# Kernel tuning notes

Hardware: AMD Instinct MI355X
Metric: run time of the kernel (lower is better)

Reference implementation:

```python
import jax, jax.numpy as jnp
import numpy as np

N, E, DIM_H, H = 50000, 400000, 128, 8
D = DIM_H // H  # 16


def _ln(x, g, b, eps=1e-5):
    mu = jnp.mean(x, axis=-1, keepdims=True)
    var = jnp.var(x, axis=-1, keepdims=True)
    return (x - mu) * jax.lax.rsqrt(var + eps) * g + b


def setup_inputs() -> dict:
    key = jax.random.key(0)
    ks = jax.random.split(key, 20)
    s = 1.0 / np.sqrt(DIM_H)
    lin = lambda k, i, o: jax.random.uniform(k, (i, o), jnp.float32, -s, s)
    inp = {
        "node_feature": jax.random.normal(ks[0], (N, DIM_H), jnp.float32),
        "edge_feature": jax.random.normal(ks[1], (E, DIM_H), jnp.float32),
        "Wq": lin(ks[2], DIM_H, DIM_H), "bq": jnp.zeros((DIM_H,), jnp.float32),
        "Wk": lin(ks[3], DIM_H, DIM_H), "bk": jnp.zeros((DIM_H,), jnp.float32),
        "Wv": lin(ks[4], DIM_H, DIM_H), "bv": jnp.zeros((DIM_H,), jnp.float32),
        "We": lin(ks[5], DIM_H, DIM_H), "be": jnp.zeros((DIM_H,), jnp.float32),
        "Wg": lin(ks[6], DIM_H, DIM_H), "bg": jnp.zeros((DIM_H,), jnp.float32),
        "Wo": lin(ks[7], DIM_H, DIM_H), "bo": jnp.zeros((DIM_H,), jnp.float32),
        "Woe": lin(ks[8], DIM_H, DIM_H), "boe": jnp.zeros((DIM_H,), jnp.float32),
        "ln1_g": jnp.ones((DIM_H,), jnp.float32), "ln1_b": jnp.zeros((DIM_H,), jnp.float32),
        "ln1e_g": jnp.ones((DIM_H,), jnp.float32), "ln1e_b": jnp.zeros((DIM_H,), jnp.float32),
        "ln2_g": jnp.ones((DIM_H,), jnp.float32), "ln2_b": jnp.zeros((DIM_H,), jnp.float32),
        "W1": lin(ks[9], DIM_H, 2 * DIM_H), "b1": jnp.zeros((2 * DIM_H,), jnp.float32),
        "W2": lin(ks[10], 2 * DIM_H, DIM_H) / np.sqrt(2.0), "b2": jnp.zeros((DIM_H,), jnp.float32),
        "edge_index": jax.random.randint(ks[11], (2, E), 0, N, jnp.int32),
    }
    return inp


def reference(node_feature, edge_feature, Wq, bq, Wk, bk, Wv, bv, We, be, Wg, bg,
              Wo, bo, Woe, boe, ln1_g, ln1_b, ln1e_g, ln1e_b, ln2_g, ln2_b,
              W1, b1, W2, b2, edge_index):
    x_in, e_in = node_feature, edge_feature
    src, dst = edge_index[0], edge_index[1]
    n = x_in.shape[0]

    x = _ln(x_in, ln1_g, ln1_b)
    e = _ln(e_in, ln1e_g, ln1e_b)

    # node projections -> [N, H, D]
    q = (x @ Wq + bq).reshape(n, H, D)
    k = (x @ Wk + bk).reshape(n, H, D)
    v = (x @ Wv + bv).reshape(n, H, D)
    # edge projections -> [E, H, D]
    ea = (e @ We + be).reshape(-1, H, D)
    eg = (e @ Wg + bg).reshape(-1, H, D)

    # gather along edges: [E, H, D]
    edge_q = q[dst]
    edge_k = k[src]
    edge_v = v[src] * jax.nn.sigmoid(eg)

    s_elt = edge_q * edge_k + ea                      # [E, H, D] (also edge output)
    scores = jnp.clip(jnp.sum(s_elt, axis=-1) / np.sqrt(D), -5.0, 5.0)  # [E, H]

    # scatter-softmax over destination nodes, per head
    m = jax.ops.segment_max(scores, dst, num_segments=n)      # [N, H]
    ex = jnp.exp(scores - m[dst])                             # [E, H]
    ssum = jax.ops.segment_sum(ex, dst, num_segments=n)       # [N, H]
    alpha = ex / ssum[dst]                                    # [E, H]

    # scatter-add aggregation
    out = jax.ops.segment_sum(alpha[..., None] * edge_v, dst, num_segments=n)  # [N, H, D]
    out = out.reshape(n, H * D)

    x_out = x_in + out @ Wo + bo
    e_out = e_in + s_elt.reshape(-1, H * D) @ Woe + boe

    # FFN ('Single') with pre-norm + residual
    h = _ln(x_out, ln2_g, ln2_b)
    x_out = x_out + jax.nn.relu(h @ W1 + b1) @ W2 + b2
    return x_out, e_out
```

## Files before the change

kernel.cpp:

```cpp
#include <hip/hip_runtime.h>

#define NN 50000
#define NE 400000
#define CAP 64
#define PACKN (7*16384 + 32768 + 32768)
#define PACKN2 (PACKN + 32768)
#define PACKB ((PACKN2 + 255)/256)

typedef unsigned int u32;
typedef unsigned short u16;
typedef __attribute__((ext_vector_type(8))) short short8;
typedef __attribute__((ext_vector_type(4))) float f32x4;
typedef __attribute__((ext_vector_type(4))) unsigned int u32x4;

union FragU { uint4 u; short8 s; };
union Chunk { uint4 v[4]; u32 d[16]; };

__device__ __forceinline__ float bflo(u32 w){ union{u32 i; float f;} v; v.i = w<<16; return v.f; }
__device__ __forceinline__ float bfhi(u32 w){ union{u32 i; float f;} v; v.i = w & 0xffff0000u; return v.f; }
__device__ __forceinline__ u32 packbf(float a, float b){
  union{float f;u32 i;} x, y; x.f=a; y.f=b;
  u32 xi = x.i + (((x.i>>16)&1u) + 0x7fffu);
  u32 yi = y.i + (((y.i>>16)&1u) + 0x7fffu);
  return (xi>>16) | (yi & 0xffff0000u);
}

#define BAR() do { \
  asm volatile("s_waitcnt lgkmcnt(0)" ::: "memory"); \
  __builtin_amdgcn_s_barrier(); \
  asm volatile("" ::: "memory"); \
} while(0)

__device__ __forceinline__ int swz64(int row, int cp){ return row*64 + (cp ^ ((row&7)<<2)); }

__device__ __forceinline__ void stage_ln(const float* __restrict__ src, long base, long nrows,
                                         const float* __restrict__ gam, const float* __restrict__ bet,
                                         u32* __restrict__ tile, int t)
{
  int row = t>>2, sub = t&3;
  bool valid = (base + row) < nrows;
  const float* p = src + (base+row)*128 + sub*32;
  float4 x[8];
  float s=0.f, s2=0.f;
  #pragma unroll
  for(int q=0;q<8;++q){
    x[q] = valid ? *(const float4*)(p + 4*q) : make_float4(0.f,0.f,0.f,0.f);
    s  += x[q].x + x[q].y + x[q].z + x[q].w;
    s2 += x[q].x*x[q].x + x[q].y*x[q].y + x[q].z*x[q].z + x[q].w*x[q].w;
  }
  s  += __shfl_xor(s,1);  s  += __shfl_xor(s,2);
  s2 += __shfl_xor(s2,1); s2 += __shfl_xor(s2,2);
  float mu  = s*(1.f/128.f);
  float var = fmaxf(s2*(1.f/128.f) - mu*mu, 0.f);
  float rs  = rsqrtf(var + 1e-5f);
  const float* gp = gam + sub*32; const float* bp = bet + sub*32;
  #pragma unroll
  for(int m4=0;m4<4;++m4){
    float4 g0 = *(const float4*)(gp + 8*m4);
    float4 g1 = *(const float4*)(gp + 8*m4 + 4);
    float4 b0 = *(const float4*)(bp + 8*m4);
    float4 b1 = *(const float4*)(bp + 8*m4 + 4);
    float4 xa = x[2*m4], xb = x[2*m4+1];
    uint4 wv;
    wv.x = packbf((xa.x-mu)*rs*g0.x+b0.x, (xa.y-mu)*rs*g0.y+b0.y);
    wv.y = packbf((xa.z-mu)*rs*g0.z+b0.z, (xa.w-mu)*rs*g0.w+b0.w);
    wv.z = packbf((xb.x-mu)*rs*g1.x+b1.x, (xb.y-mu)*rs*g1.y+b1.y);
    wv.w = packbf((xb.z-mu)*rs*g1.z+b1.z, (xb.w-mu)*rs*g1.w+b1.w);
    *(uint4*)&tile[swz64(row, sub*16 + m4*4)] = wv;
  }
}

__device__ __forceinline__ void stage_ln8(const float* __restrict__ src, long base,
                                          const float* __restrict__ gam, const float* __restrict__ bet,
                                          u32* __restrict__ tile, int t)
{
  int row = t>>3, sub = t&7;
  const float* p = src + (base+row)*128 + sub*16;
  float4 x[4];
  float s=0.f, s2=0.f;
  #pragma unroll
  for(int q=0;q<4;++q){
    x[q] = *(const float4*)(p + 4*q);
    s  += x[q].x + x[q].y + x[q].z + x[q].w;
    s2 += x[q].x*x[q].x + x[q].y*x[q].y + x[q].z*x[q].z + x[q].w*x[q].w;
  }
  s  += __shfl_xor(s,1);  s  += __shfl_xor(s,2);  s  += __shfl_xor(s,4);
  s2 += __shfl_xor(s2,1); s2 += __shfl_xor(s2,2); s2 += __shfl_xor(s2,4);
  float mu  = s*(1.f/128.f);
  float var = fmaxf(s2*(1.f/128.f) - mu*mu, 0.f);
  float rs  = rsqrtf(var + 1e-5f);
  const float* gp = gam + sub*16; const float* bp = bet + sub*16;
  #pragma unroll
  for(int m4=0;m4<2;++m4){
    float4 g0 = *(const float4*)(gp + 8*m4);
    float4 g1 = *(const float4*)(gp + 8*m4 + 4);
    float4 b0 = *(const float4*)(bp + 8*m4);
    float4 b1 = *(const float4*)(bp + 8*m4 + 4);
    float4 xa = x[2*m4], xb = x[2*m4+1];
    uint4 wv;
    wv.x = packbf((xa.x-mu)*rs*g0.x+b0.x, (xa.y-mu)*rs*g0.y+b0.y);
    wv.y = packbf((xa.z-mu)*rs*g0.z+b0.z, (xa.w-mu)*rs*g0.w+b0.w);
    wv.z = packbf((xb.x-mu)*rs*g1.x+b1.x, (xb.y-mu)*rs*g1.y+b1.y);
    wv.w = packbf((xb.z-mu)*rs*g1.z+b1.z, (xb.w-mu)*rs*g1.w+b1.w);
    *(uint4*)&tile[swz64(row, sub*8 + m4*4)] = wv;
  }
}

__device__ __forceinline__ void gemmT8(const u16* __restrict__ PW, int NT, int mtoff,
                                       const u32* __restrict__ tile, int row, int l,
                                       f32x4 acc[8])
{
  int g = l>>4;
  #pragma unroll
  for(int kc=0;kc<4;++kc){
    FragU bf; bf.u = *(const uint4*)&tile[swz64(row, kc*16 + g*4)];
    #pragma unroll
    for(int mt=0;mt<8;++mt){
      FragU af; af.u = ((const uint4*)PW)[(size_t)(kc*NT + mtoff + mt)*64 + l];
      acc[mt] = __builtin_amdgcn_mfma_f32_16x16x32_bf16(af.s, bf.s, acc[mt], 0,0,0);
    }
  }
}

__device__ __forceinline__ void gemmT4(const u16* __restrict__ PW, int NT, int mtoff,
                                       const u32* __restrict__ tile, int row, int l,
                                       f32x4 acc[4])
{
  int g = l>>4;
  #pragma unroll
  for(int kc=0;kc<4;++kc){
    FragU bf; bf.u = *(const uint4*)&tile[swz64(row, kc*16 + g*4)];
    #pragma unroll
    for(int m=0;m<4;++m){
      FragU af; af.u = ((const uint4*)PW)[(size_t)(kc*NT + mtoff + m)*64 + l];
      acc[m] = __builtin_amdgcn_mfma_f32_16x16x32_bf16(af.s, bf.s, acc[m], 0,0,0);
    }
  }
}

__global__ __launch_bounds__(256)
void k_prep(const float* __restrict__ Wq, const float* __restrict__ Wk,
            const float* __restrict__ Wv, const float* __restrict__ We,
            const float* __restrict__ Wg, const float* __restrict__ Woe,
            const float* __restrict__ Wo, const float* __restrict__ W1,
            const float* __restrict__ W2, u16* __restrict__ dst,
            const int* __restrict__ eidx, int* __restrict__ cnt, int* __restrict__ elist)
{
  if (blockIdx.x < PACKB){
    int i = blockIdx.x*256 + threadIdx.x;
    const float* src; int N, idx, nt_override = -1;
    if (i < 7*16384){
      int m = i >> 14; idx = i & 16383; N=128;
      src = (m==0)?Wq:(m==1)?Wk:(m==2)?Wv:(m==3)?We:(m==4)?Wg:(m==5)?Woe:Wo;
    } else if (i < 7*16384 + 32768){ idx = i - 7*16384; N=256; src = W1; }
    else if (i < PACKN){ idx = i - 7*16384 - 32768; N=128; src = W2; }
    else if (i < PACKN2){
      idx = i - PACKN; N=128;
      int rest = idx >> 9;
      int T = rest & 15;
      int half = T>>3, within = T&7;
      nt_override = half*4 + (within&3);
      src = (within>>2) ? Wg : We;
    }
    else return;
    int j = idx & 7, l = (idx>>3) & 63;
    int rest = idx >> 9;
    int NT = (nt_override >= 0) ? 16 : (N >> 4);
    int nt = (nt_override >= 0) ? nt_override : (rest % NT);
    int kc = rest / NT;
    int k = kc*32 + (l>>4)*8 + j;
    int n = nt*16 + (l&15);
    union{float f;u32 u;} x; x.f = src[(size_t)k*N + n];
    dst[i] = (u16)((x.u + (((x.u>>16)&1u) + 0x7fffu)) >> 16);
  } else {
    int e = (blockIdx.x - PACKB)*256 + threadIdx.x;
    if (e < NE){
      int d = eidx[NE+e];
      int pos = atomicAdd(&cnt[d], 1);
      if (pos < CAP) elist[(size_t)d*CAP + pos] = e;
    }
  }
}

__global__ __launch_bounds__(256)
void k_qkv(const float* __restrict__ xin,
           const float* __restrict__ l1g, const float* __restrict__ l1b,
           const u16* __restrict__ pWq, const float* __restrict__ bq,
           const u16* __restrict__ pWk, const float* __restrict__ bk,
           const u16* __restrict__ pWv, const float* __restrict__ bv,
           u32* __restrict__ qv, u32* __restrict__ kv, u32* __restrict__ vv)
{
  __shared__ u32 tile[64*64];
  int t = threadIdx.x;
  long base = (long)blockIdx.x * 64;
  stage_ln(xin, base, NN, l1g, l1b, tile, t);
  BAR();
  int w = t>>6, l = t&63, g = l>>4;
  int row = w*16 + (l&15);
  long node = base + row;
  bool valid = node < NN;

  f32x4 acc[8];
  const u16* pws[3] = {pWq, pWk, pWv};
  const float* bbs[3] = {bq, bk, bv};
  u32* outs[3] = {qv, kv, vv};
  #pragma unroll
  for(int s3=0;s3<3;++s3){
    #pragma unroll
    for(int mt=0;mt<8;++mt) acc[mt] = (f32x4){0.f,0.f,0.f,0.f};
    gemmT8(pws[s3], 8, 0, tile, row, l, acc);
    if (valid){
      Chunk c;
      #pragma unroll
      for(int mt=0;mt<8;++mt){
        float4 bb = *(const float4*)(bbs[s3] + mt*16 + g*4);
        c.d[mt*2]   = packbf(acc[mt][0]+bb.x, acc[mt][1]+bb.y);
        c.d[mt*2+1] = packbf(acc[mt][2]+bb.z, acc[mt][3]+bb.w);
      }
      uint4* op = (uint4*)(outs[s3] + node*64 + g*16);
      #pragma unroll
      for(int i=0;i<4;++i) op[i] = c.v[i];
    }
  }
}

__global__ __launch_bounds__(512)
void k_edge(const float* __restrict__ ein,
            const float* __restrict__ l1eg, const float* __restrict__ l1eb,
            const u16* __restrict__ pWeg, const float* __restrict__ bg,
            const float* __restrict__ be,
            const u16* __restrict__ pWoe, const float* __restrict__ boe,
            const int* __restrict__ eidx,
            const u32* __restrict__ qv, const u32* __restrict__ kv, const u32* __restrict__ vv,
            u32* __restrict__ gvp, float* __restrict__ escp,
            float* __restrict__ eout)
{
  __shared__ u32 tile[64*64];
  __shared__ u32 stile[64*64];
  int t = threadIdx.x;
  long base = (long)blockIdx.x * 64;
  stage_ln8(ein, base, l1eg, l1eb, tile, t);

  int w = t>>6, l = t&63, g = l>>4;
  int rg = w&3, half = w>>2;
  int row = rg*16 + (l&15);
  long edge = base + row;
  int s_ = eidx[edge], d_ = eidx[NE + edge];
  BAR();

  float4 er[4];
  #pragma unroll
  for(int m=0;m<4;++m)
    er[m] = *(const float4*)(ein + edge*128 + (half*4+m)*16 + g*4);
  const uint4* qp = (const uint4*)(qv + (size_t)d_*64 + g*16 + half*8);
  const uint4* kp = (const uint4*)(kv + (size_t)s_*64 + g*16 + half*8);
  const uint4* vp = (const uint4*)(vv + (size_t)s_*64 + g*16 + half*8);
  uint4 qa = qp[0], qb = qp[1];
  uint4 ka = kp[0], kb = kp[1];
  uint4 va = vp[0], vb = vp[1];
  uint2 qw[4] = {{qa.x,qa.y},{qa.z,qa.w},{qb.x,qb.y},{qb.z,qb.w}};
  uint2 kw[4] = {{ka.x,ka.y},{ka.z,ka.w},{kb.x,kb.y},{kb.z,kb.w}};
  uint2 vw[4] = {{va.x,va.y},{va.z,va.w},{vb.x,vb.y},{vb.z,vb.w}};

  f32x4 acc8[8];
  #pragma unroll
  for(int m=0;m<8;++m) acc8[m] = (f32x4){0.f,0.f,0.f,0.f};
  gemmT8(pWeg, 16, half*8, tile, row, l, acc8);

  float esc4[4];
  #pragma unroll
  for(int m=0;m<4;++m){
    int mt = half*4 + m;
    float4 bb = *(const float4*)(be + mt*16 + g*4);
    acc8[m][0] += bb.x + bflo(qw[m].x)*bflo(kw[m].x);
    acc8[m][1] += bb.y + bfhi(qw[m].x)*bfhi(kw[m].x);
    acc8[m][2] += bb.z + bflo(qw[m].y)*bflo(kw[m].y);
    acc8[m][3] += bb.w + bfhi(qw[m].y)*bfhi(kw[m].y);
    uint2 o;
    o.x = packbf(acc8[m][0], acc8[m][1]);
    o.y = packbf(acc8[m][2], acc8[m][3]);
    *(uint2*)&stile[swz64(row, mt*8 + g*2)] = o;
    float ps = acc8[m][0]+acc8[m][1]+acc8[m][2]+acc8[m][3];
    ps += __shfl_xor(ps, 16);
    ps += __shfl_xor(ps, 32);
    float sc = fminf(fmaxf(ps*0.25f, -5.f), 5.f);
    esc4[m] = __expf(sc);
  }
  if (g==0){
    float4 e0 = {esc4[0],esc4[1],esc4[2],esc4[3]};
    *(float4*)(escp + (size_t)edge*8 + half*4) = e0;
  }
  {
    u32 gd[8];
    #pragma unroll
    for(int m=0;m<4;++m){
      int mt = half*4 + m;
      float4 bb = *(const float4*)(bg + mt*16 + g*4);
      float g0 = 1.f/(1.f+__expf(-(acc8[4+m][0]+bb.x)));
      float g1 = 1.f/(1.f+__expf(-(acc8[4+m][1]+bb.y)));
      float g2 = 1.f/(1.f+__expf(-(acc8[4+m][2]+bb.z)));
      float g3 = 1.f/(1.f+__expf(-(acc8[4+m][3]+bb.w)));
      gd[m*2]   = packbf(g0*bflo(vw[m].x), g1*bfhi(vw[m].x));
      gd[m*2+1] = packbf(g2*bflo(vw[m].y), g3*bfhi(vw[m].y));
    }
    u32x4* gp2 = (u32x4*)(gvp + (size_t)edge*64 + half*32 + g*8);
    u32x4 g0v = {gd[0],gd[1],gd[2],gd[3]};
    u32x4 g1v = {gd[4],gd[5],gd[6],gd[7]};
    __builtin_nontemporal_store(g0v, gp2);
    __builtin_nontemporal_store(g1v, gp2+1);
  }
  BAR();
  f32x4 oac[4];
  #pragma unroll
  for(int m=0;m<4;++m) oac[m] = (f32x4){0.f,0.f,0.f,0.f};
  gemmT4(pWoe, 8, half*4, stile, row, l, oac);
  #pragma unroll
  for(int m=0;m<4;++m){
    int mt = half*4 + m;
    float4 bb = *(const float4*)(boe + mt*16 + g*4);
    f32x4 o;
    o[0] = er[m].x + oac[m][0] + bb.x;
    o[1] = er[m].y + oac[m][1] + bb.y;
    o[2] = er[m].z + oac[m][2] + bb.z;
    o[3] = er[m].w + oac[m][3] + bb.w;
    __builtin_nontemporal_store(o, (f32x4*)(eout + edge*128 + mt*16 + g*4));
  }
}

__global__ __launch_bounds__(256)
void k_agg(const u32* __restrict__ gvp, const float* __restrict__ escp,
           const int* __restrict__ elist, const int* __restrict__ cnt,
           u32* __restrict__ xattnb)
{
  int w = threadIdx.x>>6, l = threadIdx.x&63;
  long n = (long)blockIdx.x*4 + w;
  if (n >= NN) return;
  int h = ((l>>5)<<2) | ((l>>1)&3);
  int e = min(cnt[n], CAP);
  const int* el = elist + (size_t)n*CAP;
  float s0=0.f, s1=0.f, den=0.f;
  int i = 0;
  for (; i+8<=e; i+=8){
    int ed[8];
    #pragma unroll
    for(int j=0;j<8;++j) ed[j] = el[i+j];
    u32 gw[8]; float a[8];
    #pragma unroll
    for(int j=0;j<8;++j){ gw[j] = gvp[(size_t)ed[j]*64 + l]; a[j] = escp[(size_t)ed[j]*8 + h]; }
    #pragma unroll
    for(int j=0;j<8;++j){ s0 += a[j]*bflo(gw[j]); s1 += a[j]*bfhi(gw[j]); den += a[j]; }
  }
  if (i < e){
    int m = e - i;
    int ed[7]; u32 gw[7]; float a[7];
    #pragma unroll
    for(int j=0;j<7;++j) if (j < m) ed[j] = el[i+j];
    #pragma unroll
    for(int j=0;j<7;++j) if (j < m){ gw[j] = gvp[(size_t)ed[j]*64 + l]; a[j] = escp[(size_t)ed[j]*8 + h]; }
    #pragma unroll
    for(int j=0;j<7;++j) if (j < m){ s0 += a[j]*bflo(gw[j]); s1 += a[j]*bfhi(gw[j]); den += a[j]; }
  }
  float inv = den>0.f ? 1.f/den : 0.f;
  xattnb[n*64 + l] = packbf(s0*inv, s1*inv);
}

__global__ __launch_bounds__(256)
void k_out(const float* __restrict__ xin,
           const u32* __restrict__ xattnb,
           const u16* __restrict__ pWo, const float* __restrict__ bo,
           const float* __restrict__ l2g, const float* __restrict__ l2b,
           const u16* __restrict__ pW1, const float* __restrict__ b1p,
           const u16* __restrict__ pW2, const float* __restrict__ b2p,
           float* __restrict__ xout)
{
  __shared__ u32 tile[64*64];
  __shared__ u32 hhalf[64*64];
  int t = threadIdx.x;
  long base = (long)blockIdx.x * 64;
  {
    int row = t>>2, sub = t&3;
    long node = base + row;
    bool valid = node < NN;
    Chunk c;
    if (valid){
      const uint4* p = (const uint4*)(xattnb + node*64 + sub*16);
      #pragma unroll
      for(int i=0;i<4;++i) c.v[i] = p[i];
    } else {
      #pragma unroll
      for(int i=0;i<16;++i) c.d[i] = 0;
    }
    int half = sub>>1;
    #pragma unroll
    for(int p=0;p<8;++p){
      int g = (sub&1)*2 + (p>>2);
      int m = p&3;
      int cp = (half*4 + m)*8 + g*2;
      uint2 o; o.x = c.d[2*p]; o.y = c.d[2*p+1];
      *(uint2*)&tile[swz64(row, cp)] = o;
    }
  }
  BAR();
  int w = t>>6, l = t&63, g = l>>4;
  int row = w*16 + (l&15);
  long node = base + row;
  bool valid = node < NN;

  float4 xr[8];
  #pragma unroll
  for(int mt=0;mt<8;++mt)
    xr[mt] = valid ? *(const float4*)(xin + node*128 + mt*16 + g*4) : make_float4(0.f,0.f,0.f,0.f);

  f32x4 acc[8], xm[8];
  #pragma unroll
  for(int mt=0;mt<8;++mt) acc[mt] = (f32x4){0.f,0.f,0.f,0.f};
  gemmT8(pWo, 8, 0, tile, row, l, acc);
  #pragma unroll
  for(int mt=0;mt<8;++mt){
    float4 bb = *(const float4*)(bo + mt*16 + g*4);
    xm[mt][0] = xr[mt].x + acc[mt][0] + bb.x;
    xm[mt][1] = xr[mt].y + acc[mt][1] + bb.y;
    xm[mt][2] = xr[mt].z + acc[mt][2] + bb.z;
    xm[mt][3] = xr[mt].w + acc[mt][3] + bb.w;
  }
  float s=0.f, s2=0.f;
  #pragma unroll
  for(int mt=0;mt<8;++mt){
    s  += xm[mt][0]+xm[mt][1]+xm[mt][2]+xm[mt][3];
    s2 += xm[mt][0]*xm[mt][0]+xm[mt][1]*xm[mt][1]+xm[mt][2]*xm[mt][2]+xm[mt][3]*xm[mt][3];
  }
  s  += __shfl_xor(s,16);  s  += __shfl_xor(s,32);
  s2 += __shfl_xor(s2,16); s2 += __shfl_xor(s2,32);
  float mu  = s*(1.f/128.f);
  float var = fmaxf(s2*(1.f/128.f) - mu*mu, 0.f);
  float rs  = rsqrtf(var + 1e-5f);
  BAR();
  #pragma unroll
  for(int mt=0;mt<8;++mt){
    float4 gg = *(const float4*)(l2g + mt*16 + g*4);
    float4 bb = *(const float4*)(l2b + mt*16 + g*4);
    float h0 = (xm[mt][0]-mu)*rs*gg.x + bb.x;
    float h1 = (xm[mt][1]-mu)*rs*gg.y + bb.y;
    float h2 = (xm[mt][2]-mu)*rs*gg.z + bb.z;
    float h3 = (xm[mt][3]-mu)*rs*gg.w + bb.w;
    uint2 o; o.x = packbf(h0,h1); o.y = packbf(h2,h3);
    *(uint2*)&tile[swz64(row, mt*8 + g*2)] = o;
  }
  BAR();
  f32x4 oacc[8];
  #pragma unroll
  for(int mt=0;mt<8;++mt) oacc[mt] = (f32x4){0.f,0.f,0.f,0.f};
  #pragma unroll
  for(int hf=0; hf<2; ++hf){
    f32x4 dh[8];
    #pragma unroll
    for(int mt=0;mt<8;++mt) dh[mt] = (f32x4){0.f,0.f,0.f,0.f};
    gemmT8(pW1, 16, hf*8, tile, row, l, dh);
    #pragma unroll
    for(int mt=0;mt<8;++mt){
      int feat = hf*128 + mt*16 + g*4;
      float4 bb = *(const float4*)(b1p + feat);
      float h0 = fmaxf(dh[mt][0]+bb.x, 0.f);
      float h1 = fmaxf(dh[mt][1]+bb.y, 0.f);
      float h2 = fmaxf(dh[mt][2]+bb.z, 0.f);
      float h3 = fmaxf(dh[mt][3]+bb.w, 0.f);
      uint2 o; o.x = packbf(h0,h1); o.y = packbf(h2,h3);
      *(uint2*)&hhalf[swz64(row, mt*8 + g*2)] = o;
    }
    BAR();
    gemmT8(pW2 + (size_t)hf*16384, 8, 0, hhalf, row, l, oacc);
    BAR();
  }
  if (valid){
    #pragma unroll
    for(int mt=0;mt<8;++mt){
      float4 bb = *(const float4*)(b2p + mt*16 + g*4);
      f32x4 o;
      o[0] = xm[mt][0] + oacc[mt][0] + bb.x;
      o[1] = xm[mt][1] + oacc[mt][1] + bb.y;
      o[2] = xm[mt][2] + oacc[mt][2] + bb.z;
      o[3] = xm[mt][3] + oacc[mt][3] + bb.w;
      __builtin_nontemporal_store(o, (f32x4*)(xout + node*128 + mt*16 + g*4));
    }
  }
}

extern "C" void kernel_launch(void* const* d_in, const int* in_sizes, int n_in,
                              void* d_out, int out_size, void* d_ws, size_t ws_size,
                              hipStream_t stream) {
  (void)in_sizes; (void)n_in; (void)out_size; (void)ws_size;
  const float* xin = (const float*)d_in[0];
  const float* ein = (const float*)d_in[1];
  const float* Wq = (const float*)d_in[2];  const float* bq = (const float*)d_in[3];
  const float* Wk = (const float*)d_in[4];  const float* bk = (const float*)d_in[5];
  const float* Wv = (const float*)d_in[6];  const float* bv = (const float*)d_in[7];
  const float* We = (const float*)d_in[8];  const float* be = (const float*)d_in[9];
  const float* Wg = (const float*)d_in[10]; const float* bg = (const float*)d_in[11];
  const float* Wo = (const float*)d_in[12]; const float* bo = (const float*)d_in[13];
  const float* Woe= (const float*)d_in[14]; const float* boe= (const float*)d_in[15];
  const float* l1g= (const float*)d_in[16]; const float* l1b= (const float*)d_in[17];
  const float* l1eg=(const float*)d_in[18]; const float* l1eb=(const float*)d_in[19];
  const float* l2g= (const float*)d_in[20]; const float* l2b= (const float*)d_in[21];
  const float* W1 = (const float*)d_in[22]; const float* b1 = (const float*)d_in[23];
  const float* W2 = (const float*)d_in[24]; const float* b2 = (const float*)d_in[25];
  const int* eidx = (const int*)d_in[26];

  float* xout = (float*)d_out;
  float* eout = xout + (size_t)NN*128;

  float* escp = (float*)d_ws;
  u32* gvp = (u32*)(escp + (size_t)NE*8);
  u32* qv = gvp + (size_t)NE*64;
  u32* kv = qv + (size_t)NN*64;
  u32* vv = kv + (size_t)NN*64;
  u32* xattnb = vv + (size_t)NN*64;
  int* cnt = (int*)(xattnb + (size_t)NN*64);
  int* elist = cnt + NN;
  u16* pw  = (u16*)(elist + (size_t)NN*CAP);
  u16* pWq = pw;            u16* pWk = pWq + 16384;  u16* pWv = pWk + 16384;
  u16* pWe = pWv + 16384;   u16* pWg = pWe + 16384;  u16* pWoe= pWg + 16384;
  u16* pWo = pWoe + 16384;  u16* pW1 = pWo + 16384;  u16* pW2 = pW1 + 32768;
  u16* pWeg = pW2 + 32768;
  (void)pWe; (void)pWg;

  hipMemsetAsync(cnt, 0, NN*sizeof(int), stream);
  k_prep<<<PACKB + (NE+255)/256, 256, 0, stream>>>(Wq,Wk,Wv,We,Wg,Woe,Wo,W1,W2, pw,
                                                   eidx, cnt, elist);

  k_qkv<<<(NN+63)/64, 256, 0, stream>>>(xin, l1g, l1b, pWq, bq, pWk, bk, pWv, bv, qv, kv, vv);
  k_edge<<<NE/64, 512, 0, stream>>>(ein, l1eg, l1eb, pWeg, bg, be, pWoe, boe,
                                    eidx, qv, kv, vv, gvp, escp, eout);
  k_agg<<<(NN+3)/4, 256, 0, stream>>>(gvp, escp, elist, cnt, xattnb);
  k_out<<<(NN+63)/64, 256, 0, stream>>>(xin, xattnb, pWo, bo, l2g, l2b,
                                        pW1, b1, pW2, b2, xout);
}
```

Measured before the change: 410.7 us.

## Fuse neighbor aggregation into output kernel, writing attention result straight to LDS

The separate k_agg kernel is removed. Its per-node weighted gather over incoming edges now runs inside k_out: each wave aggregates 16 nodes one after another and writes the packed bf16 result directly into the swizzled shared tile used by the Wo GEMM. This drops the xattnb global round trip and one kernel launch. In exchange, each block's aggregation is serialized over 16 nodes per wave with less parallelism (782 blocks instead of 12500), which may hurt latency hiding for the irregular gathers.

```diff
diff --git a/kernel.cpp b/kernel.cpp
--- a/kernel.cpp
+++ b/kernel.cpp
@@ -328,45 +328,9 @@
 }
 
 __global__ __launch_bounds__(256)
-void k_agg(const u32* __restrict__ gvp, const float* __restrict__ escp,
+void k_out(const float* __restrict__ xin,
+           const u32* __restrict__ gvp, const float* __restrict__ escp,
            const int* __restrict__ elist, const int* __restrict__ cnt,
-           u32* __restrict__ xattnb)
-{
-  int w = threadIdx.x>>6, l = threadIdx.x&63;
-  long n = (long)blockIdx.x*4 + w;
-  if (n >= NN) return;
-  int h = ((l>>5)<<2) | ((l>>1)&3);
-  int e = min(cnt[n], CAP);
-  const int* el = elist + (size_t)n*CAP;
-  float s0=0.f, s1=0.f, den=0.f;
-  int i = 0;
-  for (; i+8<=e; i+=8){
-    int ed[8];
-    #pragma unroll
-    for(int j=0;j<8;++j) ed[j] = el[i+j];
-    u32 gw[8]; float a[8];
-    #pragma unroll
-    for(int j=0;j<8;++j){ gw[j] = gvp[(size_t)ed[j]*64 + l]; a[j] = escp[(size_t)ed[j]*8 + h]; }
-    #pragma unroll
-    for(int j=0;j<8;++j){ s0 += a[j]*bflo(gw[j]); s1 += a[j]*bfhi(gw[j]); den += a[j]; }
-  }
-  if (i < e){
-    int m = e - i;
-    int ed[7]; u32 gw[7]; float a[7];
-    #pragma unroll
-    for(int j=0;j<7;++j) if (j < m) ed[j] = el[i+j];
-    #pragma unroll
-    for(int j=0;j<7;++j) if (j < m){ gw[j] = gvp[(size_t)ed[j]*64 + l]; a[j] = escp[(size_t)ed[j]*8 + h]; }
-    #pragma unroll
-    for(int j=0;j<7;++j) if (j < m){ s0 += a[j]*bflo(gw[j]); s1 += a[j]*bfhi(gw[j]); den += a[j]; }
-  }
-  float inv = den>0.f ? 1.f/den : 0.f;
-  xattnb[n*64 + l] = packbf(s0*inv, s1*inv);
-}
-
-__global__ __launch_bounds__(256)
-void k_out(const float* __restrict__ xin,
-           const u32* __restrict__ xattnb,
            const u16* __restrict__ pWo, const float* __restrict__ bo,
            const float* __restrict__ l2g, const float* __restrict__ l2b,
            const u16* __restrict__ pW1, const float* __restrict__ b1p,
@@ -377,31 +341,45 @@
   __shared__ u32 hhalf[64*64];
   int t = threadIdx.x;
   long base = (long)blockIdx.x * 64;
+  int w = t>>6, l = t&63, g = l>>4;
   {
-    int row = t>>2, sub = t&3;
-    long node = base + row;
-    bool valid = node < NN;
-    Chunk c;
-    if (valid){
-      const uint4* p = (const uint4*)(xattnb + node*64 + sub*16);
-      #pragma unroll
-      for(int i=0;i<4;++i) c.v[i] = p[i];
-    } else {
-      #pragma unroll
-      for(int i=0;i<16;++i) c.d[i] = 0;
-    }
-    int half = sub>>1;
-    #pragma unroll
-    for(int p=0;p<8;++p){
-      int g = (sub&1)*2 + (p>>2);
-      int m = p&3;
-      int cp = (half*4 + m)*8 + g*2;
-      uint2 o; o.x = c.d[2*p]; o.y = c.d[2*p+1];
-      *(uint2*)&tile[swz64(row, cp)] = o;
+    int half2 = l>>5, gg2 = (l>>3)&3, m2 = (l>>1)&3, j2 = l&1;
+    int h  = half2*4 + m2;
+    int cp = (half2*4 + m2)*8 + gg2*2 + j2;
+    for (int i=0;i<16;++i){
+      int rrow = w*16 + i;
+      long node = base + rrow;
+      float s0=0.f, s1=0.f, den=0.f;
+      if (node < NN){
+        int e = min(cnt[node], CAP);
+        const int* el = elist + (size_t)node*CAP;
+        int ii = 0;
+        for (; ii+8<=e; ii+=8){
+          int ed[8];
+          #pragma unroll
+          for(int j=0;j<8;++j) ed[j] = el[ii+j];
+          u32 gw[8]; float a[8];
+          #pragma unroll
+          for(int j=0;j<8;++j){ gw[j] = gvp[(size_t)ed[j]*64 + l]; a[j] = escp[(size_t)ed[j]*8 + h]; }
+          #pragma unroll
+          for(int j=0;j<8;++j){ s0 += a[j]*bflo(gw[j]); s1 += a[j]*bfhi(gw[j]); den += a[j]; }
+        }
+        if (ii < e){
+          int mm = e - ii;
+          int ed[7]; u32 gw[7]; float a[7];
+          #pragma unroll
+          for(int j=0;j<7;++j) if (j < mm) ed[j] = el[ii+j];
+          #pragma unroll
+          for(int j=0;j<7;++j) if (j < mm){ gw[j] = gvp[(size_t)ed[j]*64 + l]; a[j] = escp[(size_t)ed[j]*8 + h]; }
+          #pragma unroll
+          for(int j=0;j<7;++j) if (j < mm){ s0 += a[j]*bflo(gw[j]); s1 += a[j]*bfhi(gw[j]); den += a[j]; }
+        }
+      }
+      float inv = den>0.f ? 1.f/den : 0.f;
+      tile[swz64(rrow, cp)] = packbf(s0*inv, s1*inv);
     }
   }
   BAR();
-  int w = t>>6, l = t&63, g = l>>4;
   int row = w*16 + (l&15);
   long node = base + row;
   bool valid = node < NN;
@@ -513,8 +491,7 @@
   u32* qv = gvp + (size_t)NE*64;
   u32* kv = qv + (size_t)NN*64;
   u32* vv = kv + (size_t)NN*64;
-  u32* xattnb = vv + (size_t)NN*64;
-  int* cnt = (int*)(xattnb + (size_t)NN*64);
+  int* cnt = (int*)(vv + (size_t)NN*64);
   int* elist = cnt + NN;
   u16* pw  = (u16*)(elist + (size_t)NN*CAP);
   u16* pWq = pw;            u16* pWk = pWq + 16384;  u16* pWv = pWk + 16384;
@@ -530,7 +507,6 @@
   k_qkv<<<(NN+63)/64, 256, 0, stream>>>(xin, l1g, l1b, pWq, bq, pWk, bk, pWv, bv, qv, kv, vv);
   k_edge<<<NE/64, 512, 0, stream>>>(ein, l1eg, l1eb, pWeg, bg, be, pWoe, boe,
                                     eidx, qv, kv, vv, gvp, escp, eout);
-  k_agg<<<(NN+3)/4, 256, 0, stream>>>(gvp, escp, elist, cnt, xattnb);
-  k_out<<<(NN+63)/64, 256, 0, stream>>>(xin, xattnb, pWo, bo, l2g, l2b,
+  k_out<<<(NN+63)/64, 256, 0, stream>>>(xin, gvp, escp, elist, cnt, pWo, bo, l2g, l2b,
                                         pW1, b1, pW2, b2, xout);
 }
```

Result: slower. 465.9 us (+13.4%).
